# Performance work log

Measured on AMD Instinct MI355X. Metric: run time of the kernel, lower is better.

The kernel has to match this reference:

```python
import jax, jax.numpy as jnp
import numpy as np

# LDPC Tanner-graph dimensions
N, M, COL_DEG = 4096, 2048, 3          # variables, checks, variable degree
E = N * COL_DEG                         # edges = 12288 (check degree = E/M = 6)
B = 128                                 # batch of codewords
T = 30                                  # BP iterations
LLR_CLIP = 15.0
MAX_WEIGHT = 1.0
RATE = 0.5
EPS = 1e-6
MIN_ABS = float(-np.log(np.tanh(LLR_CLIP / 2.0)))  # small positive lower clamp


def atanh(x, eps=EPS):
    x = x * (1.0 - eps)
    return 0.5 * jnp.log((1.0 + x) / (1.0 - x))


def two_layer(x, W1, b1, W2, b2):
    # TwoLayerNet: relu(linear1) -> sigmoid(linear2)
    h = jnp.maximum(x @ W1.T + b1, 0.0)
    return jax.nn.sigmoid(h @ W2.T + b2)


def setup_inputs() -> dict:
    key = jax.random.key(0)
    ks = jax.random.split(key, 8)
    rng = np.random.default_rng(0)
    # Regular LDPC edge list: each variable appears COL_DEG times; a random
    # permutation mod M gives every check exactly E/M = 6 edges.
    col_idx = jnp.asarray(np.repeat(np.arange(N), COL_DEG), dtype=jnp.int32)
    row_idx = jnp.asarray(rng.permutation(E) % M, dtype=jnp.int32)
    chn_llr = jax.random.normal(ks[0], (N, B), dtype=jnp.float32) * 4.0
    p = lambda k, s: (jax.random.normal(k, s, dtype=jnp.float32) * 0.5)
    return {
        "chn_llr": chn_llr,
        "gW1": p(ks[1], (20, 1)), "gb1": jnp.zeros((20,), jnp.float32),
        "gW2": p(ks[2], (1, 20)), "gb2": jnp.zeros((1,), jnp.float32),
        "iW1": p(ks[3], (20, 1)), "ib1": jnp.zeros((20,), jnp.float32),
        "iW2": p(ks[4], (1, 20)), "ib2": jnp.zeros((1,), jnp.float32),
        "eW1": p(ks[5], (20, 1)), "eb1": jnp.zeros((20,), jnp.float32),
        "eW2": p(ks[6], (1, 20)), "eb2": jnp.zeros((1,), jnp.float32),
        "row_idx": row_idx,
        "col_idx": col_idx,
    }


def reference(chn_llr, gW1, gb1, gW2, gb2, iW1, ib1, iW2, ib2,
              eW1, eb1, eW2, eb2, row_idx, col_idx):
    # --- adaptive parameter nets on estimated SNR (est_SNR=True path) ---
    Eng = jnp.mean(chn_llr ** 2, axis=0)                       # (B,)
    snr_hat = 10.0 * jnp.log10(Eng / (1.0 + jnp.sqrt(1.0 + Eng)) / (4.0 * RATE))
    x = snr_hat[:, None]                                        # (B,1)
    gamma = two_layer(x, gW1, gb1, gW2, gb2).T                  # (1,B)
    Wi = MAX_WEIGHT * two_layer(x, iW1, ib1, iW2, ib2).T        # (1,B)
    We = MAX_WEIGHT * two_layer(x, eW1, eb1, eW2, eb2).T        # (1,B)

    seg_col = lambda v: jax.ops.segment_sum(v, col_idx, num_segments=N)  # (N,B)
    seg_row = lambda v: jax.ops.segment_sum(v, row_idx, num_segments=M)  # (M,B)
    col_sum_loo = lambda v: seg_col(v)[col_idx] - v             # leave-one-out over columns
    row_sum_loo = lambda v: seg_row(v)[row_idx] - v             # leave-one-out over rows

    ell_w = Wi * chn_llr                                        # (N,B), Wi*ell reused

    def step(carry, _):
        msg_V2C, msg_C2V = carry                                # each (E,B)
        # V step: llr_int + llr_ext, then damping
        v_new = ell_w[col_idx] + col_sum_loo(We * msg_C2V)
        msg_V2C = (1.0 - gamma) * msg_V2C + gamma * v_new
        # H step: sign-magnitude tanh/atanh form, then damping
        lam = jnp.clip(msg_V2C, -LLR_CLIP, LLR_CLIP)
        neg_cnt = row_sum_loo((lam < 0).astype(lam.dtype))
        sgn = jnp.where(jnp.mod(neg_cnt, 2.0) > 0.5, -1.0, 1.0)
        abs_lam = jnp.clip(jnp.abs(lam), MIN_ABS, LLR_CLIP)
        amp = row_sum_loo(jnp.log(jnp.tanh(abs_lam / 2.0)))
        c_new = sgn * 2.0 * atanh(jnp.exp(amp))
        msg_C2V = (1.0 - gamma) * msg_C2V + gamma * c_new
        # M step: marginal soft output (N,B)
        out = ell_w + seg_col(We * msg_C2V)
        return (msg_V2C, msg_C2V), out

    init = (jnp.zeros((E, B), chn_llr.dtype), jnp.zeros((E, B), chn_llr.dtype))
    _, outs = jax.lax.scan(step, init, None, length=T)          # (T,N,B)
    return outs
```

## Files before the change

kernel.cpp:

```cpp
#include <hip/hip_runtime.h>
#include <cstddef>


namespace {
constexpr int N  = 4096;
constexpr int M  = 2048;
constexpr int CD = 3;
constexpr int RD = 6;
constexpr int E  = N * CD;
constexpr int B  = 128;
constexpr int T  = 30;
constexpr float CLIP    = 15.0f;
constexpr float FEPS    = 1e-6f;
constexpr float MIN_ABS = 6.1180465e-07f;
constexpr int TPB = 1024;
constexpr int VPT = N / TPB;
constexpr int CPT = M / TPB;

__global__ __launch_bounds__(256) void k_build(const int* __restrict__ row_idx,
                                               int* __restrict__ cnt,
                                               int* __restrict__ vlist) {
  int e = blockIdx.x * 256 + threadIdx.x;
  if (e < E) {
    int m    = row_idx[e];
    int slot = atomicAdd(&cnt[m], 1);
    vlist[e] = slot * M + m;
  }
}

__global__ __launch_bounds__(TPB, 4) void k_fused(
    const float* __restrict__ chn,
    const float* __restrict__ gW1, const float* __restrict__ gb1,
    const float* __restrict__ gW2, const float* __restrict__ gb2,
    const float* __restrict__ iW1, const float* __restrict__ ib1,
    const float* __restrict__ iW2, const float* __restrict__ ib2,
    const float* __restrict__ eW1, const float* __restrict__ eb1,
    const float* __restrict__ eW2, const float* __restrict__ eb2,
    const int* __restrict__ vlist, float* __restrict__ outT) {
  __shared__ float us_s[RD * M];
  __shared__ float c2v_s[RD * M];
  __shared__ float red[32];

  const int tid  = threadIdx.x;
  const int b    = blockIdx.x;
  const int wid  = tid >> 6;
  const int lane = tid & 63;

  for (int i = tid; i < RD * M; i += TPB) c2v_s[i] = 0.f;

  float ch[VPT];
  float local = 0.f;
#pragma unroll
  for (int i = 0; i < VPT; ++i) {
    int v = tid + i * TPB;
    ch[i] = chn[(size_t)v * B + b];
    local += ch[i] * ch[i];
  }
#pragma unroll
  for (int off = 32; off > 0; off >>= 1) local += __shfl_down(local, off, 64);
  if (lane == 0) red[wid] = local;
  __syncthreads();
  if (tid == 0) {
    float tot = 0.f;
    for (int w = 0; w < 16; ++w) tot += red[w];
    red[16] = tot * (1.f / (float)N);
  }
  __syncthreads();
  if (wid < 3) {
    float Eng = red[16];
    float snr = 10.f * log10f(Eng / (1.f + sqrtf(1.f + Eng)) * 0.5f);
    const float *W1, *b1, *W2, *b2;
    if (wid == 0)      { W1 = gW1; b1 = gb1; W2 = gW2; b2 = gb2; }
    else if (wid == 1) { W1 = iW1; b1 = ib1; W2 = iW2; b2 = ib2; }
    else               { W1 = eW1; b1 = eb1; W2 = eW2; b2 = eb2; }
    float h = 0.f;
    if (lane < 20) h = fmaxf(snr * W1[lane] + b1[lane], 0.f) * W2[lane];
#pragma unroll
    for (int off = 32; off > 0; off >>= 1) h += __shfl_down(h, off, 64);
    if (lane == 0) red[20 + wid] = 1.f / (1.f + expf(-(h + b2[0])));
  }
  __syncthreads();
  const float g   = red[20];
  const float wiv = red[21];
  const float wev = red[22];
  const float omg = 1.f - g;
  float ell[VPT];
#pragma unroll
  for (int i = 0; i < VPT; ++i) ell[i] = wiv * ch[i];

  int vl[VPT][CD];
#pragma unroll
  for (int i = 0; i < VPT; ++i) {
    int v = tid + i * TPB;
#pragma unroll
    for (int j = 0; j < CD; ++j) vl[i][j] = vlist[v * CD + j];
  }
  float v2c[VPT][CD] = {};
  float c2v[CPT][RD] = {};
  __syncthreads();

#define VAR_EDGE(i, J, WJ)                                              \
  {                                                                     \
    float nv  = fmaf(omg, v2c[i][J], g * (es - (WJ)));                  \
    v2c[i][J] = nv;                                                     \
    float l   = fminf(fmaxf(nv, -CLIP), CLIP);                          \
    float al  = fmaxf(fabsf(l), MIN_ABS);                               \
    float u   = 2.f * __builtin_amdgcn_rcpf(__expf(al) + 1.f);          \
    us_s[vl[i][J]] = (l < 0.f) ? -u : u;    \
  }

  for (int t = 0; t < T; ++t) {
#pragma unroll
    for (int i = 0; i < VPT; ++i) {
      int v    = tid + i * TPB;
      float w0 = c2v_s[vl[i][0]];
      float w1 = c2v_s[vl[i][1]];
      float w2 = c2v_s[vl[i][2]];
      float es = ell[i] + ((w0 + w1) + w2);
      if (t > 0) outT[((size_t)b * T + (t - 1)) * N + v] = es;
      VAR_EDGE(i, 0, w0)
      VAR_EDGE(i, 1, w1)
      VAR_EDGE(i, 2, w2)
    }
    __syncthreads();
#pragma unroll
    for (int i = 0; i < CPT; ++i) {
      int m = tid + i * TPB;
      float u[RD], tt[RD];
      unsigned int sb[RD], s_all = 0u;
#pragma unroll
      for (int k = 0; k < RD; ++k) {
        float usv = us_s[k * M + m];
        float a   = fabsf(usv);
        u[k]  = a;
        tt[k] = 1.f - a;
        sb[k] = __float_as_uint(usv) & 0x80000000u;
        s_all ^= sb[k];
      }
      float omp[RD + 1], Pp[RD + 1];
      omp[0] = 0.f; Pp[0] = 1.f;
#pragma unroll
      for (int k = 0; k < RD; ++k) {
        omp[k + 1] = fmaf(Pp[k], u[k], omp[k]);
        Pp[k + 1]  = Pp[k] * tt[k];
      }
      float oms = 0.f, Ps = 1.f;
#pragma unroll
      for (int k = RD - 1; k >= 0; --k) {
        float om_loo = fmaf(Pp[k], oms, omp[k]);
        float P_loo  = Pp[k] * Ps;
        float den  = fmaf(FEPS, P_loo, om_loo);
        float num  = 2.f - den;
        float cnew = __logf(num * __builtin_amdgcn_rcpf(den));
        cnew = __uint_as_float(__float_as_uint(cnew) ^ (s_all ^ sb[k]));
        float nc   = fmaf(omg, c2v[i][k], g * cnew);
        c2v[i][k]  = nc;
        c2v_s[k * M + m] = wev * nc;
        oms = fmaf(tt[k], oms, u[k]);
        Ps *= tt[k];
      }
    }
    __syncthreads();
  }
#pragma unroll
  for (int i = 0; i < VPT; ++i) {
    int v   = tid + i * TPB;
    float s = (c2v_s[vl[i][0]] + c2v_s[vl[i][1]]) + c2v_s[vl[i][2]];
    outT[((size_t)b * T + (T - 1)) * N + v] = ell[i] + s;
  }
#undef VAR_EDGE
}

__global__ __launch_bounds__(256) void k_tr(const float* __restrict__ outT,
                                            float* __restrict__ out) {
  __shared__ float tile[128 * 65];
  int t   = blockIdx.y;
  int v0  = blockIdx.x * 64;
  int tid = threadIdx.x;
#pragma unroll
  for (int r = 0; r < 32; ++r) {
    int bb = r * 4 + (tid >> 6);
    int v  = tid & 63;
    tile[bb * 65 + v] = outT[((size_t)bb * T + t) * N + v0 + v];
  }
  __syncthreads();
#pragma unroll
  for (int r = 0; r < 32; ++r) {
    int v  = r * 2 + (tid >> 7);
    int bb = tid & 127;
    __builtin_nontemporal_store(tile[bb * 65 + v],
                                &out[((size_t)t * N + v0 + v) * B + bb]);
  }
}

}

extern "C" void kernel_launch(void* const* d_in, const int* in_sizes, int n_in,
                              void* d_out, int out_size, void* d_ws,
                              size_t ws_size, hipStream_t stream) {
  const float* chn = (const float*)d_in[0];
  const float* gW1 = (const float*)d_in[1];
  const float* gb1 = (const float*)d_in[2];
  const float* gW2 = (const float*)d_in[3];
  const float* gb2 = (const float*)d_in[4];
  const float* iW1 = (const float*)d_in[5];
  const float* ib1 = (const float*)d_in[6];
  const float* iW2 = (const float*)d_in[7];
  const float* ib2 = (const float*)d_in[8];
  const float* eW1 = (const float*)d_in[9];
  const float* eb1 = (const float*)d_in[10];
  const float* eW2 = (const float*)d_in[11];
  const float* eb2 = (const float*)d_in[12];
  const int* row_idx = (const int*)d_in[13];
  float* out = (float*)d_out;

  float* outT  = (float*)d_ws;
  int*   cnt   = (int*)(outT + (size_t)B * T * N);
  int*   vlist = cnt + M;

  hipMemsetAsync(cnt, 0, M * sizeof(int), stream);
  k_build<<<(E + 255) / 256, 256, 0, stream>>>(row_idx, cnt, vlist);
  k_fused<<<B, TPB, 0, stream>>>(chn, gW1, gb1, gW2, gb2, iW1, ib1, iW2, ib2,
                                 eW1, eb1, eW2, eb2, vlist, outT);
  dim3 tg(N / 64, T);
  k_tr<<<tg, 256, 0, stream>>>(outT, out);
}
```

Measured before the change: 244.5 us.

## Merge edge buffers into check-major padded LDS rows and build slots in-kernel

Replaces the two edge-indexed shared arrays (v2c-transformed and c2v) with one check-major buffer padded to 12 floats per check. The variable step and the check step read and write the same slots in place, and check nodes load and store their 6 edges with float4/float2 vector accesses. Edge slot assignment now uses shared-memory atomics inside the fused kernel, which removes the memset and the separate build kernel launch. In exchange, the stride-12 rows may cause some LDS bank conflicts, and the launch-bounds occupancy hint was dropped.

After: 242.1 us. About the same (-1.0%).

```diff
diff --git a/kernel.cpp b/kernel.cpp
--- a/kernel.cpp
+++ b/kernel.cpp
@@ -7,9 +7,9 @@
 constexpr int M  = 2048;
 constexpr int CD = 3;
 constexpr int RD = 6;
-constexpr int E  = N * CD;
 constexpr int B  = 128;
 constexpr int T  = 30;
+constexpr int PAD = 12;
 constexpr float CLIP    = 15.0f;
 constexpr float FEPS    = 1e-6f;
 constexpr float MIN_ABS = 6.1180465e-07f;
@@ -17,18 +17,7 @@
 constexpr int VPT = N / TPB;
 constexpr int CPT = M / TPB;
 
-__global__ __launch_bounds__(256) void k_build(const int* __restrict__ row_idx,
-                                               int* __restrict__ cnt,
-                                               int* __restrict__ vlist) {
-  int e = blockIdx.x * 256 + threadIdx.x;
-  if (e < E) {
-    int m    = row_idx[e];
-    int slot = atomicAdd(&cnt[m], 1);
-    vlist[e] = slot * M + m;
-  }
-}
-
-__global__ __launch_bounds__(TPB, 4) void k_fused(
+__global__ __launch_bounds__(TPB) void k_fused(
     const float* __restrict__ chn,
     const float* __restrict__ gW1, const float* __restrict__ gb1,
     const float* __restrict__ gW2, const float* __restrict__ gb2,
@@ -36,9 +25,9 @@
     const float* __restrict__ iW2, const float* __restrict__ ib2,
     const float* __restrict__ eW1, const float* __restrict__ eb1,
     const float* __restrict__ eW2, const float* __restrict__ eb2,
-    const int* __restrict__ vlist, float* __restrict__ outT) {
-  __shared__ float us_s[RD * M];
-  __shared__ float c2v_s[RD * M];
+    const int* __restrict__ row_idx, float* __restrict__ outT) {
+  __shared__ float x_s[M * PAD];
+  __shared__ int   cnt_s[M];
   __shared__ float red[32];
 
   const int tid  = threadIdx.x;
@@ -46,7 +35,8 @@
   const int wid  = tid >> 6;
   const int lane = tid & 63;
 
-  for (int i = tid; i < RD * M; i += TPB) c2v_s[i] = 0.f;
+  for (int i = tid; i < M * PAD; i += TPB) x_s[i] = 0.f;
+  for (int i = tid; i < M; i += TPB) cnt_s[i] = 0;
 
   float ch[VPT];
   float local = 0.f;
@@ -79,6 +69,17 @@
     for (int off = 32; off > 0; off >>= 1) h += __shfl_down(h, off, 64);
     if (lane == 0) red[20 + wid] = 1.f / (1.f + expf(-(h + b2[0])));
   }
+  int vl[VPT][CD];
+#pragma unroll
+  for (int i = 0; i < VPT; ++i) {
+    int v = tid + i * TPB;
+#pragma unroll
+    for (int j = 0; j < CD; ++j) {
+      int m    = row_idx[v * CD + j];
+      int slot = atomicAdd(&cnt_s[m], 1);
+      vl[i][j] = m * PAD + slot;
+    }
+  }
   __syncthreads();
   const float g   = red[20];
   const float wiv = red[21];
@@ -88,16 +89,8 @@
 #pragma unroll
   for (int i = 0; i < VPT; ++i) ell[i] = wiv * ch[i];
 
-  int vl[VPT][CD];
-#pragma unroll
-  for (int i = 0; i < VPT; ++i) {
-    int v = tid + i * TPB;
-#pragma unroll
-    for (int j = 0; j < CD; ++j) vl[i][j] = vlist[v * CD + j];
-  }
   float v2c[VPT][CD] = {};
   float c2v[CPT][RD] = {};
-  __syncthreads();
 
 #define VAR_EDGE(i, J, WJ)                                              \
   {                                                                     \
@@ -106,16 +99,16 @@
     float l   = fminf(fmaxf(nv, -CLIP), CLIP);                          \
     float al  = fmaxf(fabsf(l), MIN_ABS);                               \
     float u   = 2.f * __builtin_amdgcn_rcpf(__expf(al) + 1.f);          \
-    us_s[vl[i][J]] = (l < 0.f) ? -u : u;    \
+    x_s[vl[i][J]] = (l < 0.f) ? -u : u;     \
   }
 
   for (int t = 0; t < T; ++t) {
 #pragma unroll
     for (int i = 0; i < VPT; ++i) {
       int v    = tid + i * TPB;
-      float w0 = c2v_s[vl[i][0]];
-      float w1 = c2v_s[vl[i][1]];
-      float w2 = c2v_s[vl[i][2]];
+      float w0 = x_s[vl[i][0]];
+      float w1 = x_s[vl[i][1]];
+      float w2 = x_s[vl[i][2]];
       float es = ell[i] + ((w0 + w1) + w2);
       if (t > 0) outT[((size_t)b * T + (t - 1)) * N + v] = es;
       VAR_EDGE(i, 0, w0)
@@ -126,15 +119,18 @@
 #pragma unroll
     for (int i = 0; i < CPT; ++i) {
       int m = tid + i * TPB;
+      float* row = &x_s[m * PAD];
+      float4 q4 = *(const float4*)row;
+      float2 q2 = *(const float2*)(row + 4);
+      float usv[RD] = {q4.x, q4.y, q4.z, q4.w, q2.x, q2.y};
       float u[RD], tt[RD];
       unsigned int sb[RD], s_all = 0u;
 #pragma unroll
       for (int k = 0; k < RD; ++k) {
-        float usv = us_s[k * M + m];
-        float a   = fabsf(usv);
+        float a = fabsf(usv[k]);
         u[k]  = a;
         tt[k] = 1.f - a;
-        sb[k] = __float_as_uint(usv) & 0x80000000u;
+        sb[k] = __float_as_uint(usv[k]) & 0x80000000u;
         s_all ^= sb[k];
       }
       float omp[RD + 1], Pp[RD + 1];
@@ -145,6 +141,7 @@
         Pp[k + 1]  = Pp[k] * tt[k];
       }
       float oms = 0.f, Ps = 1.f;
+      float wout[RD];
 #pragma unroll
       for (int k = RD - 1; k >= 0; --k) {
         float om_loo = fmaf(Pp[k], oms, omp[k]);
@@ -155,17 +152,19 @@
         cnew = __uint_as_float(__float_as_uint(cnew) ^ (s_all ^ sb[k]));
         float nc   = fmaf(omg, c2v[i][k], g * cnew);
         c2v[i][k]  = nc;
-        c2v_s[k * M + m] = wev * nc;
+        wout[k]    = wev * nc;
         oms = fmaf(tt[k], oms, u[k]);
         Ps *= tt[k];
       }
+      *(float4*)row       = make_float4(wout[0], wout[1], wout[2], wout[3]);
+      *(float2*)(row + 4) = make_float2(wout[4], wout[5]);
     }
     __syncthreads();
   }
 #pragma unroll
   for (int i = 0; i < VPT; ++i) {
     int v   = tid + i * TPB;
-    float s = (c2v_s[vl[i][0]] + c2v_s[vl[i][1]]) + c2v_s[vl[i][2]];
+    float s = (x_s[vl[i][0]] + x_s[vl[i][1]]) + x_s[vl[i][2]];
     outT[((size_t)b * T + (T - 1)) * N + v] = ell[i] + s;
   }
 #undef VAR_EDGE
@@ -214,14 +213,10 @@
   const int* row_idx = (const int*)d_in[13];
   float* out = (float*)d_out;
 
-  float* outT  = (float*)d_ws;
-  int*   cnt   = (int*)(outT + (size_t)B * T * N);
-  int*   vlist = cnt + M;
-
-  hipMemsetAsync(cnt, 0, M * sizeof(int), stream);
-  k_build<<<(E + 255) / 256, 256, 0, stream>>>(row_idx, cnt, vlist);
+  float* outT = (float*)d_ws;
+
   k_fused<<<B, TPB, 0, stream>>>(chn, gW1, gb1, gW2, gb2, iW1, ib1, iW2, ib2,
-                                 eW1, eb1, eW2, eb2, vlist, outT);
+                                 eW1, eb1, eW2, eb2, row_idx, outT);
   dim3 tg(N / 64, T);
   k_tr<<<tg, 256, 0, stream>>>(outT, out);
 }
```
